# Kernel tuning notes

Measured on AMD Instinct MI355X. Metric: run time of the kernel, lower is better.

The kernel has to match this reference:

```python
import jax, jax.numpy as jnp
import numpy as np

B, N, H = 4, 1024, 64

def setup_inputs() -> dict:
    key = jax.random.key(0)
    k1, k2, k3 = jax.random.split(key, 3)
    x = jax.random.normal(k1, (B, N, H), dtype=jnp.float32)
    # nn.Linear(2H, H): weight [H, 2H], bias [H]
    s1 = 1.0 / np.sqrt(2 * H)
    W1 = jax.random.uniform(k2, (H, 2 * H), minval=-s1, maxval=s1, dtype=jnp.float32)
    b1 = jnp.zeros((H,), dtype=jnp.float32)
    # nn.Linear(H, 1): weight [1, H], bias [1]
    s2 = 1.0 / np.sqrt(H)
    W2 = jax.random.uniform(k3, (1, H), minval=-s2, maxval=s2, dtype=jnp.float32)
    b2 = jnp.zeros((1,), dtype=jnp.float32)
    return {"x": x, "W1": W1, "b1": b1, "W2": W2, "b2": b2}

def reference(x, W1, b1, W2, b2):
    # cat([x_i, x_j]) @ W1.T == x_i @ W1a.T + x_j @ W1b.T  (decomposed; same math)
    W1a, W1b = W1[:, :x.shape[-1]], W1[:, x.shape[-1]:]
    hi = jnp.einsum('bid,hd->bih', x, W1a)            # [B,N,H]
    hj = jnp.einsum('bjd,hd->bjh', x, W1b)            # [B,N,H]
    h = jax.nn.relu(hi[:, :, None, :] + hj[:, None, :, :] + b1)  # [B,N,N,H]
    logits = jnp.einsum('bijh,h->bij', h, W2[0]) + b2[0]          # [B,N,N]
    attn = jax.nn.softmax(logits, axis=-1)
    updated = jnp.einsum('bij,bjd->bid', attn, x)     # [B,N,H]
    return updated, attn
```

## Files before the change

kernel.cpp:

```cpp
#include <hip/hip_runtime.h>

#define ATTN_OFF 262144

#define WS_HIP  0
#define WS_HJP  131072

typedef float4 f4;
typedef _Float16 h2v __attribute__((ext_vector_type(2)));

union F4H { f4 f; h2v h[4]; };
union F2H { float2 f; h2v h[2]; };

__device__ __forceinline__ f4 ld4(const float* p) { return *reinterpret_cast<const f4*>(p); }
__device__ __forceinline__ void st4(float* p, f4 v) { *reinterpret_cast<f4*>(p) = v; }
__device__ __forceinline__ float fdot2f(h2v a, h2v b, float c) {
    return __builtin_amdgcn_fdot2(a, b, c, false);
}
__device__ __forceinline__ h2v pack2(float a, float b) {
    h2v r; r.x = (_Float16)a; r.y = (_Float16)b; return r;
}

__global__ __launch_bounds__(256, 4)
void ka_proj(const float* __restrict__ x, const float* __restrict__ W1,
             const float* __restrict__ b1,
             h2v* __restrict__ hiP, h2v* __restrict__ hjP) {
    __shared__ float xT[64 * 36];
    __shared__ float w1T[64 * 68];
    const int t  = threadIdx.x;
    const int i0 = blockIdx.x * 32;
    const int b  = blockIdx.y;
    const int z  = blockIdx.z;
    const int lo = t & 15;
    const int dq = t >> 4;
#pragma unroll
    for (int p = 0; p < 2; ++p) {
        const int il = p * 16 + lo;
        f4 v = ld4(&x[(size_t)(b * 1024 + i0 + il) * 64 + dq * 4]);
        xT[(dq * 4 + 0) * 36 + il] = v.x;
        xT[(dq * 4 + 1) * 36 + il] = v.y;
        xT[(dq * 4 + 2) * 36 + il] = v.z;
        xT[(dq * 4 + 3) * 36 + il] = v.w;
    }
#pragma unroll
    for (int p = 0; p < 4; ++p) {
        const int cl = p * 16 + lo;
        f4 w = ld4(&W1[(size_t)cl * 128 + z * 64 + dq * 4]);
        w1T[(dq * 4 + 0) * 68 + cl] = w.x;
        w1T[(dq * 4 + 1) * 68 + cl] = w.y;
        w1T[(dq * 4 + 2) * 68 + cl] = w.z;
        w1T[(dq * 4 + 3) * 68 + cl] = w.w;
    }
    __syncthreads();
    const int tx = t & 15;
    const int ty = t >> 4;
    float acc[2][4];
    if (z == 0) {
        f4 bv = ld4(&b1[tx * 4]);
        acc[0][0] = acc[1][0] = bv.x;
        acc[0][1] = acc[1][1] = bv.y;
        acc[0][2] = acc[1][2] = bv.z;
        acc[0][3] = acc[1][3] = bv.w;
    } else {
#pragma unroll
        for (int ii = 0; ii < 2; ++ii)
#pragma unroll
            for (int cc = 0; cc < 4; ++cc) acc[ii][cc] = 0.f;
    }
#pragma unroll 8
    for (int d = 0; d < 64; ++d) {
        const float2 xv = *reinterpret_cast<const float2*>(&xT[d * 36 + ty * 2]);
        const f4 wv = ld4(&w1T[d * 68 + tx * 4]);
        acc[0][0] = fmaf(xv.x, wv.x, acc[0][0]);
        acc[0][1] = fmaf(xv.x, wv.y, acc[0][1]);
        acc[0][2] = fmaf(xv.x, wv.z, acc[0][2]);
        acc[0][3] = fmaf(xv.x, wv.w, acc[0][3]);
        acc[1][0] = fmaf(xv.y, wv.x, acc[1][0]);
        acc[1][1] = fmaf(xv.y, wv.y, acc[1][1]);
        acc[1][2] = fmaf(xv.y, wv.z, acc[1][2]);
        acc[1][3] = fmaf(xv.y, wv.w, acc[1][3]);
    }
    h2v* outp = z ? hjP : hiP;
#pragma unroll
    for (int p = 0; p < 2; ++p) {
        F2H uo;
        uo.h[0] = pack2(acc[0][p * 2], acc[0][p * 2 + 1]);
        uo.h[1] = pack2(acc[1][p * 2], acc[1][p * 2 + 1]);
        *reinterpret_cast<float2*>(
            &outp[(size_t)(b * 32 + tx * 2 + p) * 1024 + i0 + ty * 2]) = uo.f;
    }
}

__global__ __launch_bounds__(256, 2)
void kf_fused(const h2v* __restrict__ hiP, const h2v* __restrict__ hjP,
              const float* __restrict__ W2, const float* __restrict__ x,
              float* __restrict__ attn, float* __restrict__ upd) {
    __shared__ union __align__(16) U {
        h2v   hj[32 * 256];
        h2v   xc[128 * 68];
        float red[16 * 516];
    } u;
    __shared__ __align__(16) h2v s_p[512 * 12];
    __shared__ h2v s_hi[32 * 8];
    __shared__ h2v s_w2[32];
    __shared__ float s_il[8];

    const int t  = threadIdx.x;
    const int i0 = blockIdx.x * 8;
    const int b  = blockIdx.y;
    const int tx = t & 31;
    const int ty = t >> 5;
    {
        const int hp = t >> 3, ii8 = t & 7;
        s_hi[hp * 8 + ii8] = hiP[(size_t)(b * 32 + hp) * 1024 + i0 + ii8];
    }
    if (t < 16) {
        f4 w = ld4(&W2[t * 4]);
        s_w2[t * 2]     = pack2(w.x, w.y);
        s_w2[t * 2 + 1] = pack2(w.z, w.w);
    }
    float l[4][2][4];
#pragma unroll
    for (int c = 0; c < 4; ++c)
#pragma unroll
        for (int g = 0; g < 2; ++g)
#pragma unroll
            for (int k = 0; k < 4; ++k) l[c][g][k] = 0.f;
    const h2v z2 = (h2v)0;
#pragma unroll
    for (int c = 0; c < 4; ++c) {
#pragma unroll
        for (int p = 0; p < 8; ++p) {
            const int s = p * 256 + t;
            const int hp = s >> 6, j4 = (s & 63) * 4;
            st4((float*)&u.hj[hp * 256 + j4],
                ld4((const float*)&hjP[(size_t)(b * 32 + hp) * 1024 + c * 256 + j4]));
        }
        __syncthreads();
#pragma unroll 4
        for (int hp = 0; hp < 32; ++hp) {
            const h2v hv = s_hi[hp * 8 + ty];
            const h2v wv = s_w2[hp];
#pragma unroll
            for (int g = 0; g < 2; ++g) {
                F4H bb;
                bb.f = ld4((const float*)&u.hj[hp * 256 + g * 128 + tx * 4]);
#pragma unroll
                for (int k = 0; k < 4; ++k) {
                    h2v r = __builtin_elementwise_max(hv + bb.h[k], z2);
                    l[c][g][k] = fdot2f(r, wv, l[c][g][k]);
                }
            }
        }
        __syncthreads();
    }
    float m = l[0][0][0];
#pragma unroll
    for (int c = 0; c < 4; ++c)
#pragma unroll
        for (int g = 0; g < 2; ++g)
#pragma unroll
            for (int k = 0; k < 4; ++k) m = fmaxf(m, l[c][g][k]);
#pragma unroll
    for (int d = 1; d < 32; d <<= 1) m = fmaxf(m, __shfl_xor(m, d));
    float sum = 0.f;
#pragma unroll
    for (int c = 0; c < 4; ++c)
#pragma unroll
        for (int g = 0; g < 2; ++g)
#pragma unroll
            for (int k = 0; k < 4; ++k) {
                l[c][g][k] = __expf(l[c][g][k] - m);
                sum += l[c][g][k];
            }
#pragma unroll
    for (int d = 1; d < 32; d <<= 1) sum += __shfl_xor(sum, d);
    const float il = 1.0f / sum;
    if (tx == 0) s_il[ty] = il;
    const size_t arow = (size_t)(b * 1024 + i0 + ty) * 1024 + tx * 4;
#pragma unroll
    for (int c = 0; c < 4; ++c)
#pragma unroll
        for (int g = 0; g < 2; ++g) {
            st4(&attn[arow + c * 256 + g * 128],
                make_float4(l[c][g][0] * il, l[c][g][1] * il,
                            l[c][g][2] * il, l[c][g][3] * il));
            const int jp = c * 128 + g * 64 + tx * 2;
            s_p[jp * 12 + ty]       = pack2(l[c][g][0], l[c][g][1]);
            s_p[(jp + 1) * 12 + ty] = pack2(l[c][g][2], l[c][g][3]);
        }
    const int dq = t & 15, js = t >> 4;
    float acc[8][4];
#pragma unroll
    for (int i = 0; i < 8; ++i)
#pragma unroll
        for (int q = 0; q < 4; ++q) acc[i][q] = 0.f;
#pragma unroll
    for (int c2 = 0; c2 < 4; ++c2) {
        __syncthreads();
#pragma unroll
        for (int p = 0; p < 8; ++p) {
            const int s = p * 256 + t;
            const int jpl = s >> 4, dd = (s & 15) * 4;
            const float* xr = &x[(size_t)(b * 1024 + c2 * 256 + jpl * 2) * 64 + dd];
            f4 r0 = ld4(xr);
            f4 r1 = ld4(xr + 64);
            F4H pk;
            pk.h[0] = pack2(r0.x, r1.x); pk.h[1] = pack2(r0.y, r1.y);
            pk.h[2] = pack2(r0.z, r1.z); pk.h[3] = pack2(r0.w, r1.w);
            st4((float*)&u.xc[jpl * 68 + dd], pk.f);
        }
        __syncthreads();
#pragma unroll 2
        for (int u8 = 0; u8 < 8; ++u8) {
            const int jpl = u8 * 16 + js;
            const int jp  = c2 * 128 + jpl;
            F4H p0, p1, xv;
            p0.f = ld4((const float*)&s_p[jp * 12]);
            p1.f = ld4((const float*)&s_p[jp * 12 + 4]);
            xv.f = ld4((const float*)&u.xc[jpl * 68 + dq * 4]);
#pragma unroll
            for (int i = 0; i < 8; ++i) {
                const h2v pa = (i < 4) ? p0.h[i] : p1.h[i - 4];
#pragma unroll
                for (int q = 0; q < 4; ++q)
                    acc[i][q] = fdot2f(pa, xv.h[q], acc[i][q]);
            }
        }
    }
    __syncthreads();
#pragma unroll
    for (int i = 0; i < 8; ++i)
        st4(&u.red[js * 516 + i * 64 + dq * 4],
            make_float4(acc[i][0], acc[i][1], acc[i][2], acc[i][3]));
    __syncthreads();
    if (t < 128) {
        const int i = t >> 4, dqq = t & 15;
        f4 a = ld4(&u.red[i * 64 + dqq * 4]);
#pragma unroll
        for (int js2 = 1; js2 < 16; ++js2) {
            f4 v = ld4(&u.red[js2 * 516 + i * 64 + dqq * 4]);
            a.x += v.x; a.y += v.y; a.z += v.z; a.w += v.w;
        }
        const float sc = s_il[i];
        st4(&upd[(size_t)(b * 1024 + i0 + i) * 64 + dqq * 4],
            make_float4(a.x * sc, a.y * sc, a.z * sc, a.w * sc));
    }
}

extern "C" void kernel_launch(void* const* d_in, const int* in_sizes, int n_in,
                              void* d_out, int out_size, void* d_ws, size_t ws_size,
                              hipStream_t stream) {
    const float* x  = (const float*)d_in[0];
    const float* W1 = (const float*)d_in[1];
    const float* b1 = (const float*)d_in[2];
    const float* W2 = (const float*)d_in[3];
    float* out = (float*)d_out;
    float* ws  = (float*)d_ws;
    h2v* hiP = (h2v*)(ws + WS_HIP);
    h2v* hjP = (h2v*)(ws + WS_HJP);

    ka_proj <<<dim3(32, 4, 2), 256, 0, stream>>>(x, W1, b1, hiP, hjP);
    kf_fused<<<dim3(128, 4),   256, 0, stream>>>(hiP, hjP, W2, x, out + ATTN_OFF, out);
}
```

Baseline: 98.10 us.

## Remap logits thread tiling to wave64 with two rows per wave and registers

Changes the logits phase so each 64-lane wave handles two query rows over 256 contiguous columns instead of 32-thread groups handling one row. Each LDS load of hj is now reused for two rows, and the hi and W2 values are cached in registers once rather than reread from LDS every iteration. Softmax reductions now span the full 64-lane wave. This raises register pressure (64 extra h2v registers) under the 2-blocks-per-SM launch bound, which could hurt occupancy.

```diff
diff --git a/kernel.cpp b/kernel.cpp
--- a/kernel.cpp
+++ b/kernel.cpp
@@ -107,24 +107,25 @@
     const int t  = threadIdx.x;
     const int i0 = blockIdx.x * 8;
     const int b  = blockIdx.y;
-    const int tx = t & 31;
-    const int ty = t >> 5;
+    const int w  = t >> 6;
+    const int ln = t & 63;
     {
-        const int hp = t >> 3, ii8 = t & 7;
-        s_hi[hp * 8 + ii8] = hiP[(size_t)(b * 32 + hp) * 1024 + i0 + ii8];
+        const int hp = t >> 3, r = t & 7;
+        s_hi[hp * 8 + r] = hiP[(size_t)(b * 32 + hp) * 1024 + i0 + r];
     }
     if (t < 16) {
-        f4 w = ld4(&W2[t * 4]);
-        s_w2[t * 2]     = pack2(w.x, w.y);
-        s_w2[t * 2 + 1] = pack2(w.z, w.w);
-    }
-    float l[4][2][4];
-#pragma unroll
-    for (int c = 0; c < 4; ++c)
-#pragma unroll
-        for (int g = 0; g < 2; ++g)
-#pragma unroll
-            for (int k = 0; k < 4; ++k) l[c][g][k] = 0.f;
+        f4 wq = ld4(&W2[t * 4]);
+        s_w2[t * 2]     = pack2(wq.x, wq.y);
+        s_w2[t * 2 + 1] = pack2(wq.z, wq.w);
+    }
+    float l[2][4][4];
+#pragma unroll
+    for (int r = 0; r < 2; ++r)
+#pragma unroll
+        for (int c = 0; c < 4; ++c)
+#pragma unroll
+            for (int k = 0; k < 4; ++k) l[r][c][k] = 0.f;
+    h2v hiR[2][32], w2R[32];
     const h2v z2 = (h2v)0;
 #pragma unroll
     for (int c = 0; c < 4; ++c) {
@@ -136,58 +137,68 @@
                 ld4((const float*)&hjP[(size_t)(b * 32 + hp) * 1024 + c * 256 + j4]));
         }
         __syncthreads();
-#pragma unroll 4
+        if (c == 0) {
+#pragma unroll
+            for (int hp = 0; hp < 32; ++hp) {
+                hiR[0][hp] = s_hi[hp * 8 + w];
+                hiR[1][hp] = s_hi[hp * 8 + w + 4];
+                w2R[hp]    = s_w2[hp];
+            }
+        }
+#pragma unroll
         for (int hp = 0; hp < 32; ++hp) {
-            const h2v hv = s_hi[hp * 8 + ty];
-            const h2v wv = s_w2[hp];
-#pragma unroll
-            for (int g = 0; g < 2; ++g) {
-                F4H bb;
-                bb.f = ld4((const float*)&u.hj[hp * 256 + g * 128 + tx * 4]);
+            F4H bb;
+            bb.f = ld4((const float*)&u.hj[hp * 256 + ln * 4]);
+            const h2v wv = w2R[hp];
+#pragma unroll
+            for (int r = 0; r < 2; ++r) {
+                const h2v hv = hiR[r][hp];
 #pragma unroll
                 for (int k = 0; k < 4; ++k) {
-                    h2v r = __builtin_elementwise_max(hv + bb.h[k], z2);
-                    l[c][g][k] = fdot2f(r, wv, l[c][g][k]);
+                    h2v rr = __builtin_elementwise_max(hv + bb.h[k], z2);
+                    l[r][c][k] = fdot2f(rr, wv, l[r][c][k]);
                 }
             }
         }
         __syncthreads();
     }
-    float m = l[0][0][0];
-#pragma unroll
-    for (int c = 0; c < 4; ++c)
-#pragma unroll
-        for (int g = 0; g < 2; ++g)
-#pragma unroll
-            for (int k = 0; k < 4; ++k) m = fmaxf(m, l[c][g][k]);
-#pragma unroll
-    for (int d = 1; d < 32; d <<= 1) m = fmaxf(m, __shfl_xor(m, d));
-    float sum = 0.f;
-#pragma unroll
-    for (int c = 0; c < 4; ++c)
-#pragma unroll
-        for (int g = 0; g < 2; ++g)
+    float il[2];
+#pragma unroll
+    for (int r = 0; r < 2; ++r) {
+        float m = l[r][0][0];
+#pragma unroll
+        for (int c = 0; c < 4; ++c)
+#pragma unroll
+            for (int k = 0; k < 4; ++k) m = fmaxf(m, l[r][c][k]);
+#pragma unroll
+        for (int d = 1; d < 64; d <<= 1) m = fmaxf(m, __shfl_xor(m, d));
+        float sum = 0.f;
+#pragma unroll
+        for (int c = 0; c < 4; ++c)
 #pragma unroll
             for (int k = 0; k < 4; ++k) {
-                l[c][g][k] = __expf(l[c][g][k] - m);
-                sum += l[c][g][k];
-            }
-#pragma unroll
-    for (int d = 1; d < 32; d <<= 1) sum += __shfl_xor(sum, d);
-    const float il = 1.0f / sum;
-    if (tx == 0) s_il[ty] = il;
-    const size_t arow = (size_t)(b * 1024 + i0 + ty) * 1024 + tx * 4;
-#pragma unroll
-    for (int c = 0; c < 4; ++c)
-#pragma unroll
-        for (int g = 0; g < 2; ++g) {
-            st4(&attn[arow + c * 256 + g * 128],
-                make_float4(l[c][g][0] * il, l[c][g][1] * il,
-                            l[c][g][2] * il, l[c][g][3] * il));
-            const int jp = c * 128 + g * 64 + tx * 2;
-            s_p[jp * 12 + ty]       = pack2(l[c][g][0], l[c][g][1]);
-            s_p[(jp + 1) * 12 + ty] = pack2(l[c][g][2], l[c][g][3]);
-        }
+                l[r][c][k] = __expf(l[r][c][k] - m);
+                sum += l[r][c][k];
+            }
+#pragma unroll
+        for (int d = 1; d < 64; d <<= 1) sum += __shfl_xor(sum, d);
+        il[r] = 1.0f / sum;
+    }
+    if (ln == 0) { s_il[w] = il[0]; s_il[w + 4] = il[1]; }
+#pragma unroll
+    for (int r = 0; r < 2; ++r) {
+        const int row = w + r * 4;
+        const size_t arow = (size_t)(b * 1024 + i0 + row) * 1024 + ln * 4;
+#pragma unroll
+        for (int c = 0; c < 4; ++c) {
+            st4(&attn[arow + c * 256],
+                make_float4(l[r][c][0] * il[r], l[r][c][1] * il[r],
+                            l[r][c][2] * il[r], l[r][c][3] * il[r]));
+            const int jp = c * 128 + ln * 2;
+            s_p[jp * 12 + row]       = pack2(l[r][c][0], l[r][c][1]);
+            s_p[(jp + 1) * 12 + row] = pack2(l[r][c][2], l[r][c][3]);
+        }
+    }
     const int dq = t & 15, js = t >> 4;
     float acc[8][4];
 #pragma unroll
```

Result: no change. 99.16 us (+1.1%).
